# Kernel tuning notes

Measured on AMD Instinct MI355X. Metric: run time of the kernel, lower is better.

The kernel has to match this reference:

```python
import jax, jax.numpy as jnp
import numpy as np

B, N, H, D, L = 2, 256, 256, 64, 6  # batch, pocket atoms, hidden dim, atom feat dim, EGNN layers


def _lin(x, w, b):
    return x @ w + b


def setup_inputs() -> dict:
    key = jax.random.key(0)
    ks = iter(jax.random.split(key, 64))

    def w(shape, s=0.05):
        return jax.random.normal(next(ks), shape, jnp.float32) * s

    inp = {
        'pocket_coords': jax.random.normal(next(ks), (B, N, 3), jnp.float32),
        'pocket_features': jax.random.normal(next(ks), (B, N, D), jnp.float32),
        't': jax.random.uniform(next(ks), (B,), jnp.float32, 0.0, 1000.0),
        'pe_w1': w((3 + D, H)), 'pe_b1': w((H,)),
        'pe_w2': w((H, H)), 'pe_b2': w((H,)),
        'pe_w3': w((H, H)), 'pe_b3': w((H,)),
        'te_w1': w((1, H)), 'te_b1': w((H,)),
        'te_w2': w((H, H)), 'te_b2': w((H,)),
        'ln_g': jnp.ones((L, H), jnp.float32), 'ln_b': jnp.zeros((L, H), jnp.float32),
        'ew1': w((L, 2 * H + 1, H)), 'eb1': w((L, H)),
        'ew2': w((L, H, H)), 'eb2': w((L, H)),
        'cw1': w((L, H, H)), 'cb1': w((L, H)),
        'cw2': w((L, H, 1)), 'cb2': w((L, 1)),
        'nw1': w((L, 2 * H, H)), 'nb1': w((L, H)),
        'nw2': w((L, H, H)), 'nb2': w((L, H)),
        'dec_w1': w((H, H)), 'dec_b1': w((H,)),
        'dec_w2': w((H, H)), 'dec_b2': w((H,)),
        'dec_w3': w((H, 3)), 'dec_b3': w((3,)),
    }
    return inp


def reference(pocket_coords, pocket_features, t,
              pe_w1, pe_b1, pe_w2, pe_b2, pe_w3, pe_b3,
              te_w1, te_b1, te_w2, te_b2,
              ln_g, ln_b,
              ew1, eb1, ew2, eb2,
              cw1, cb1, cw2, cb2,
              nw1, nb1, nw2, nb2,
              dec_w1, dec_b1, dec_w2, dec_b2, dec_w3, dec_b3):
    relu, silu = jax.nn.relu, jax.nn.silu

    # --- pocket encoder (residual MLP; in_dim 67 != H so no skip; dropout = identity at eval)
    pin = jnp.concatenate([pocket_coords, pocket_features], axis=-1)  # [B,N,3+D]
    h = relu(_lin(pin, pe_w1, pe_b1))
    h = relu(_lin(h, pe_w2, pe_b2))
    h = relu(_lin(h, pe_w3, pe_b3))

    # --- time embedding, broadcast over atoms
    te = relu(_lin(t[:, None], te_w1, te_b1))
    te = _lin(te, te_w2, te_b2)  # [B,H]
    h = h + te[:, None, :]

    # --- 6-layer dense EGNN (all-pairs), norm_feats=True -> LayerNorm on h per layer
    x = pocket_coords
    for l in range(L):
        h_in = h
        mu = h.mean(-1, keepdims=True)
        hc = h - mu
        hn = hc / jnp.sqrt((hc * hc).mean(-1, keepdims=True) + 1e-5) * ln_g[l] + ln_b[l]
        rel = x[:, :, None, :] - x[:, None, :, :]            # [B,N,N,3]
        d2 = jnp.sum(rel * rel, axis=-1, keepdims=True)      # [B,N,N,1]
        hi = jnp.broadcast_to(hn[:, :, None, :], (B, N, N, H))
        hj = jnp.broadcast_to(hn[:, None, :, :], (B, N, N, H))
        eij = jnp.concatenate([hi, hj, d2], axis=-1)         # [B,N,N,2H+1]
        m = silu(_lin(eij, ew1[l], eb1[l]))
        m = silu(_lin(m, ew2[l], eb2[l]))                    # [B,N,N,H] messages
        cw = _lin(silu(_lin(m, cw1[l], cb1[l])), cw2[l], cb2[l])  # [B,N,N,1]
        x = x + jnp.mean(rel * cw, axis=2)                   # equivariant coord update
        magg = jnp.sum(m, axis=2)                            # [B,N,H] aggregated messages
        u = silu(_lin(jnp.concatenate([hn, magg], axis=-1), nw1[l], nb1[l]))
        h = h_in + _lin(u, nw2[l], nb2[l])                   # residual node update

    # --- decoder (residual MLP, dims equal so skip applies before final projection)
    o = relu(_lin(h, dec_w1, dec_b1))
    o = relu(_lin(o, dec_w2, dec_b2)) + h
    return _lin(o, dec_w3, dec_b3)                           # predicted noise [B,N,3]
```

## Files before the change

kernel.cpp:

```cpp
#include <hip/hip_runtime.h>
#include <math.h>

static constexpr int NB = 2, NN = 256, HH = 256, DD = 64, LL = 6;
static constexpr int RN = NB * NN * HH;
static constexpr int SROWB = 528;

typedef __attribute__((ext_vector_type(8))) short bf16x8;
typedef __attribute__((ext_vector_type(4))) float f32x4;
typedef __attribute__((ext_vector_type(4))) float float4v;
typedef __attribute__((ext_vector_type(4))) unsigned int u32x4;

__device__ __forceinline__ float fsilu(float v) {
    return v * __builtin_amdgcn_rcpf(1.0f + __expf(-v));
}
__device__ __forceinline__ unsigned short f2bf(float f) {
    union { float f; unsigned int u; } x; x.f = f;
    unsigned int r = x.u + 0x7fffu + ((x.u >> 16) & 1u);
    return (unsigned short)(r >> 16);
}
__device__ __forceinline__ float bitsf(unsigned int u) {
    union { float f; unsigned int u; } x; x.u = u; return x.f;
}
__device__ __forceinline__ float bflo(unsigned int w) { return bitsf(w << 16); }
__device__ __forceinline__ float bfhi(unsigned int w) { return bitsf(w & 0xffff0000u); }
__device__ __forceinline__ unsigned int cvtpk(float lo, float hi) {
    unsigned int w;
    asm("v_cvt_pk_bf16_f32 %0, %1, %2" : "=v"(w) : "v"(lo), "v"(hi));
    return w;
}

__global__ void k_convert(const float* __restrict__ ew2, const float* __restrict__ cw1,
                          unsigned short* __restrict__ ew2P, unsigned short* __restrict__ cw1P) {
    int g = blockIdx.x * blockDim.x + threadIdx.x;
    if (g >= LL * 8192) return;
    int l = g >> 13;
    int r = g & 8191;
    int lane = r & 63;
    int fidx = r >> 6;
    int ks = fidx >> 4;
    int wv = (fidx >> 1) & 7;
    int ct = fidx & 1;
    int col = wv * 32 + ct * 16 + (lane & 15);
    int k0 = ks * 32 + (lane >> 4) * 8;
    #pragma unroll
    for (int e = 0; e < 8; ++e) {
        ew2P[(size_t)g * 8 + e] = f2bf(ew2[((size_t)l * HH + k0 + e) * HH + col]);
        cw1P[(size_t)g * 8 + e] = f2bf(cw1[((size_t)l * HH + k0 + e) * HH + col]);
    }
}

__global__ void k_convert2(const float* __restrict__ nw1, const float* __restrict__ nw2,
                           const float* __restrict__ ew1,
                           unsigned short* __restrict__ nw1B, unsigned short* __restrict__ nw2B,
                           unsigned short* __restrict__ ew1B) {
    int idx = blockIdx.x * blockDim.x + threadIdx.x;
    if (idx >= LL * 131072) return;
    int l = idx >> 17;
    int r = idx & 131071;
    int c = r >> 8, col = r & 255;
    int dst = (l << 17) + ((c >> 1) << 9) + (col << 1) + (c & 1);
    nw1B[dst] = f2bf(nw1[(size_t)l * 131072 + c * 256 + col]);
    ew1B[dst] = f2bf(ew1[(size_t)l * 131328 + c * 256 + col]);
    if (r < 65536) {
        int d2 = (l << 16) + ((c >> 1) << 9) + (col << 1) + (c & 1);
        nw2B[d2] = f2bf(nw2[(size_t)l * 65536 + c * 256 + col]);
    }
}

__global__ __launch_bounds__(256) void k_encoder(
    const float* __restrict__ coords, const float* __restrict__ feats, const float* __restrict__ t,
    const float* __restrict__ pw1, const float* __restrict__ pb1,
    const float* __restrict__ pw2, const float* __restrict__ pb2,
    const float* __restrict__ pw3, const float* __restrict__ pb3,
    const float* __restrict__ tw1, const float* __restrict__ tb1,
    const float* __restrict__ tw2, const float* __restrict__ tb2,
    float* __restrict__ h, float* __restrict__ x) {
    __shared__ float spinT[68][2];
    __shared__ float shaT[HH][2];
    __shared__ float shbT[HH][2];
    __shared__ float ste1[HH];
    int tid = threadIdx.x;
    int base = blockIdx.x * 2;
    int b = base / NN;

    #pragma unroll
    for (int r = 0; r < 2; ++r) {
        int row = base + r;
        if (tid < 3) spinT[tid][r] = coords[row * 3 + tid];
        if (tid < DD) spinT[3 + tid][r] = feats[row * DD + tid];
    }
    float tv = t[b];
    ste1[tid] = fmaxf(tv * tw1[tid] + tb1[tid], 0.0f);
    if (tid < 6) {
        int r = tid / 3, c = tid % 3;
        x[(base + r) * 3 + c] = coords[(base + r) * 3 + c];
    }
    __syncthreads();

    float a0 = pb1[tid], a1 = a0;
    for (int c = 0; c < 67; ++c) {
        float w = pw1[c * HH + tid];
        float2 s = *(const float2*)&spinT[c][0];
        a0 += s.x * w; a1 += s.y * w;
    }
    shaT[tid][0] = fmaxf(a0, 0.f); shaT[tid][1] = fmaxf(a1, 0.f);
    __syncthreads();
    a0 = pb2[tid]; a1 = a0;
    for (int c = 0; c < HH; ++c) {
        float w = pw2[c * HH + tid];
        float2 s = *(const float2*)&shaT[c][0];
        a0 += s.x * w; a1 += s.y * w;
    }
    shbT[tid][0] = fmaxf(a0, 0.f); shbT[tid][1] = fmaxf(a1, 0.f);
    __syncthreads();
    a0 = pb3[tid]; a1 = a0;
    float te = tb2[tid];
    for (int c = 0; c < HH; ++c) {
        float w = pw3[c * HH + tid];
        float2 s = *(const float2*)&shbT[c][0];
        a0 += s.x * w; a1 += s.y * w;
        te += ste1[c] * tw2[c * HH + tid];
    }
    h[(base + 0) * HH + tid] = fmaxf(a0, 0.f) + te;
    h[(base + 1) * HH + tid] = fmaxf(a1, 0.f) + te;
}

__global__ __launch_bounds__(256) void k_ln_aiaj(
    const float* __restrict__ h, const float* __restrict__ g, const float* __restrict__ bta,
    const unsigned int* __restrict__ ew1w, const float* __restrict__ eb1l,
    float* __restrict__ hn, float* __restrict__ Ai, unsigned short* __restrict__ AjB) {
    __shared__ float shnT[HH][2];
    int tid = threadIdx.x, wv = tid >> 6, lane = tid & 63;
    int base = blockIdx.x * 2;

    if (wv < 2) {
        int row = base + wv;
        float v[4];
        #pragma unroll
        for (int q = 0; q < 4; ++q) v[q] = h[row * HH + lane + 64 * q];
        float s = v[0] + v[1] + v[2] + v[3];
        #pragma unroll
        for (int m = 1; m < 64; m <<= 1) s += __shfl_xor(s, m);
        float mu = s * (1.0f / HH);
        float var = 0.f;
        #pragma unroll
        for (int q = 0; q < 4; ++q) { v[q] -= mu; var += v[q] * v[q]; }
        #pragma unroll
        for (int m = 1; m < 64; m <<= 1) var += __shfl_xor(var, m);
        float rstd = rsqrtf(var * (1.0f / HH) + 1e-5f);
        #pragma unroll
        for (int q = 0; q < 4; ++q) {
            int k = lane + 64 * q;
            float hv = v[q] * rstd * g[k] + bta[k];
            shnT[k][wv] = hv;
            hn[row * HH + k] = hv;
        }
    }
    __syncthreads();

    float ai0a = eb1l[tid], ai1a = ai0a, ai0b = 0.f, ai1b = 0.f;
    float aj0a = 0.f, aj1a = 0.f, aj0b = 0.f, aj1b = 0.f;
    #pragma unroll 4
    for (int c2 = 0; c2 < 128; c2 += 2) {
        unsigned int wipA = ew1w[c2 * 256 + tid];
        unsigned int wjpA = ew1w[(128 + c2) * 256 + tid];
        unsigned int wipB = ew1w[(c2 + 1) * 256 + tid];
        unsigned int wjpB = ew1w[(129 + c2) * 256 + tid];
        float4 sA = *(const float4*)&shnT[c2 * 2][0];
        float4 sB = *(const float4*)&shnT[c2 * 2 + 2][0];
        ai0a += sA.x * bflo(wipA) + sA.z * bfhi(wipA);
        ai1a += sA.y * bflo(wipA) + sA.w * bfhi(wipA);
        aj0a += sA.x * bflo(wjpA) + sA.z * bfhi(wjpA);
        aj1a += sA.y * bflo(wjpA) + sA.w * bfhi(wjpA);
        ai0b += sB.x * bflo(wipB) + sB.z * bfhi(wipB);
        ai1b += sB.y * bflo(wipB) + sB.w * bfhi(wipB);
        aj0b += sB.x * bflo(wjpB) + sB.z * bfhi(wjpB);
        aj1b += sB.y * bflo(wjpB) + sB.w * bfhi(wjpB);
    }
    Ai[(base + 0) * HH + tid] = ai0a + ai0b; AjB[(base + 0) * HH + tid] = f2bf(aj0a + aj0b);
    Ai[(base + 1) * HH + tid] = ai1a + ai1b; AjB[(base + 1) * HH + tid] = f2bf(aj1a + aj1b);
}

__global__ __launch_bounds__(512, 1) void k_edge(
    const float* __restrict__ x, const float* __restrict__ Ai, const unsigned short* __restrict__ AjB,
    const float* __restrict__ wd, const float* __restrict__ eb2v,
    const unsigned short* __restrict__ ew2P, const unsigned short* __restrict__ cw1P,
    const float* __restrict__ cb1v, const float* __restrict__ cw2v, const float* __restrict__ cb2p,
    float* __restrict__ h, float* __restrict__ hn,
    float* __restrict__ xnext, float* __restrict__ Ainext, unsigned short* __restrict__ AjBnext,
    const unsigned int* __restrict__ nw1w, const float* __restrict__ nb1l,
    const unsigned int* __restrict__ nw2w, const float* __restrict__ nb2l,
    const float* __restrict__ gamv, const float* __restrict__ betv,
    const unsigned int* __restrict__ ew1wn, const float* __restrict__ eb1n,
    int has_ln) {
    __shared__ float cwpart[8][128];
    __shared__ float smagg2[2][256];
    __shared__ __attribute__((aligned(16))) char s_tile[128 * SROWB];
    __shared__ __attribute__((aligned(16))) char m_tile[128 * SROWB];

    int tid = threadIdx.x, wv = tid >> 6, lane = tid & 63;
    int g4 = lane >> 4, l15 = lane & 15;
    int colbase = wv * 32;
    int ni0 = blockIdx.x * 2;
    int ni1 = ni0 + 1;
    int b = ni0 >> 8;
    int bbase = b * NN;
    int bthr = ((wv << 7) + lane) << 3;
    int k0p = (tid & 31) << 3;

    float wdv[8];
    {
        float4v w0 = *(const float4v*)(wd + k0p);
        float4v w1 = *(const float4v*)(wd + k0p + 4);
        #pragma unroll
        for (int e = 0; e < 4; ++e) { wdv[e] = w0[e]; wdv[4 + e] = w1[e]; }
    }
    float eb2r[2], cb1r[2], cw2r[2];
    #pragma unroll
    for (int ct = 0; ct < 2; ++ct) {
        int col = colbase + ct * 16 + l15;
        eb2r[ct] = eb2v[col]; cb1r[ct] = cb1v[col]; cw2r[ct] = cw2v[col];
    }
    float cb2 = cb2p[0];

    bf16x8 Bew[8][2], Bcw[8][2];
    #pragma unroll
    for (int ks = 0; ks < 8; ++ks) {
        #pragma unroll
        for (int ct = 0; ct < 2; ++ct) {
            Bew[ks][ct] = *(const bf16x8*)(ew2P + (ks << 13) + (ct << 9) + bthr);
            Bcw[ks][ct] = *(const bf16x8*)(cw1P + (ks << 13) + (ct << 9) + bthr);
        }
    }

    char* p1w = s_tile + ((tid >> 5) * SROWB + k0p * 2);
    const char* aA = s_tile + (l15 * SROWB + g4 * 16);
    const char* aM = m_tile + (l15 * SROWB + g4 * 16);
    char* mwA = m_tile + ((g4 * 4) * SROWB + (colbase + l15) * 2);

    #pragma unroll 1
    for (int ir = 0; ir < 2; ++ir) {
        int ni = ni0 + ir;
        float aiv[8];
        {
            float4v a0 = *(const float4v*)(Ai + (size_t)ni * HH + k0p);
            float4v a1 = *(const float4v*)(Ai + (size_t)ni * HH + k0p + 4);
            #pragma unroll
            for (int e = 0; e < 4; ++e) { aiv[e] = a0[e]; aiv[4 + e] = a1[e]; }
        }
        float xi0 = x[ni * 3 + 0], xi1 = x[ni * 3 + 1], xi2 = x[ni * 3 + 2];
        float mgv[2] = {0.f, 0.f};
        float xd0 = 0.f, xd1 = 0.f, xd2 = 0.f;

        #pragma unroll 1
        for (int jc = 0; jc < 2; ++jc) {
            int j0 = jc * 128;
            __syncthreads();

            #pragma unroll
            for (int it = 0; it < 8; ++it) {
                int row = it * 16 + (tid >> 5);
                int j = bbase + j0 + row;
                float rx = xi0 - x[j * 3 + 0];
                float ry = xi1 - x[j * 3 + 1];
                float rz = xi2 - x[j * 3 + 2];
                float d2v = rx * rx + ry * ry + rz * rz;
                u32x4 ajw = *(const u32x4*)(AjB + ((size_t)j * HH + k0p));
                unsigned int uw0, uw1, uw2, uw3;
                uw0 = cvtpk(fsilu(aiv[0] + bflo(ajw[0]) + d2v * wdv[0]), fsilu(aiv[1] + bfhi(ajw[0]) + d2v * wdv[1]));
                uw1 = cvtpk(fsilu(aiv[2] + bflo(ajw[1]) + d2v * wdv[2]), fsilu(aiv[3] + bfhi(ajw[1]) + d2v * wdv[3]));
                uw2 = cvtpk(fsilu(aiv[4] + bflo(ajw[2]) + d2v * wdv[4]), fsilu(aiv[5] + bfhi(ajw[2]) + d2v * wdv[5]));
                uw3 = cvtpk(fsilu(aiv[6] + bflo(ajw[3]) + d2v * wdv[6]), fsilu(aiv[7] + bfhi(ajw[3]) + d2v * wdv[7]));
                u32x4 sv = {uw0, uw1, uw2, uw3};
                *reinterpret_cast<u32x4*>(p1w + it * 16 * SROWB) = sv;
            }
            __syncthreads();

            #pragma unroll 1
            for (int rh = 0; rh < 4; ++rh) {
                f32x4 acc[2][2];
                acc[0][0] = (f32x4){0.f,0.f,0.f,0.f}; acc[0][1] = (f32x4){0.f,0.f,0.f,0.f};
                acc[1][0] = (f32x4){0.f,0.f,0.f,0.f}; acc[1][1] = (f32x4){0.f,0.f,0.f,0.f};
                const char* aBase = aA + rh * 32 * SROWB;
                #pragma unroll
                for (int ks = 0; ks < 8; ++ks) {
                    bf16x8 a0 = *reinterpret_cast<const bf16x8*>(aBase + ks * 64);
                    bf16x8 a1 = *reinterpret_cast<const bf16x8*>(aBase + 16 * SROWB + ks * 64);
                    acc[0][0] = __builtin_amdgcn_mfma_f32_16x16x32_bf16(a0, Bew[ks][0], acc[0][0], 0, 0, 0);
                    acc[0][1] = __builtin_amdgcn_mfma_f32_16x16x32_bf16(a0, Bew[ks][1], acc[0][1], 0, 0, 0);
                    acc[1][0] = __builtin_amdgcn_mfma_f32_16x16x32_bf16(a1, Bew[ks][0], acc[1][0], 0, 0, 0);
                    acc[1][1] = __builtin_amdgcn_mfma_f32_16x16x32_bf16(a1, Bew[ks][1], acc[1][1], 0, 0, 0);
                }
                char* mw = mwA + rh * 32 * SROWB;
                #pragma unroll
                for (int rt = 0; rt < 2; ++rt) {
                    #pragma unroll
                    for (int r = 0; r < 4; ++r) {
                        float v0 = fsilu(acc[rt][0][r] + eb2r[0]);
                        float v1 = fsilu(acc[rt][1][r] + eb2r[1]);
                        mgv[0] += v0; mgv[1] += v1;
                        unsigned int w = cvtpk(v0, v1);
                        char* p = mw + (rt * 16 + r) * SROWB;
                        *reinterpret_cast<unsigned short*>(p) = (unsigned short)w;
                        *reinterpret_cast<unsigned short*>(p + 32) = (unsigned short)(w >> 16);
                    }
                }
            }
            __syncthreads();

            #pragma unroll 1
            for (int rh = 0; rh < 4; ++rh) {
                f32x4 acc[2][2];
                acc[0][0] = (f32x4){0.f,0.f,0.f,0.f}; acc[0][1] = (f32x4){0.f,0.f,0.f,0.f};
                acc[1][0] = (f32x4){0.f,0.f,0.f,0.f}; acc[1][1] = (f32x4){0.f,0.f,0.f,0.f};
                const char* aBase = aM + rh * 32 * SROWB;
                #pragma unroll
                for (int ks = 0; ks < 8; ++ks) {
                    bf16x8 a0 = *reinterpret_cast<const bf16x8*>(aBase + ks * 64);
                    bf16x8 a1 = *reinterpret_cast<const bf16x8*>(aBase + 16 * SROWB + ks * 64);
                    acc[0][0] = __builtin_amdgcn_mfma_f32_16x16x32_bf16(a0, Bcw[ks][0], acc[0][0], 0, 0, 0);
                    acc[0][1] = __builtin_amdgcn_mfma_f32_16x16x32_bf16(a0, Bcw[ks][1], acc[0][1], 0, 0, 0);
                    acc[1][0] = __builtin_amdgcn_mfma_f32_16x16x32_bf16(a1, Bcw[ks][0], acc[1][0], 0, 0, 0);
                    acc[1][1] = __builtin_amdgcn_mfma_f32_16x16x32_bf16(a1, Bcw[ks][1], acc[1][1], 0, 0, 0);
                }
                float rs[8];
                #pragma unroll
                for (int q = 0; q < 8; ++q) rs[q] = 0.f;
                #pragma unroll
                for (int ct = 0; ct < 2; ++ct) {
                    #pragma unroll
                    for (int rt = 0; rt < 2; ++rt)
                        #pragma unroll
                        for (int r = 0; r < 4; ++r)
                            rs[rt * 4 + r] += fsilu(acc[rt][ct][r] + cb1r[ct]) * cw2r[ct];
                }
                #pragma unroll
                for (int m = 1; m <= 8; m <<= 1)
                    #pragma unroll
                    for (int q = 0; q < 8; ++q) rs[q] += __shfl_xor(rs[q], m);
                if (l15 == 0) {
                    #pragma unroll
                    for (int rt = 0; rt < 2; ++rt)
                        #pragma unroll
                        for (int r = 0; r < 4; ++r)
                            cwpart[wv][rh * 32 + rt * 16 + g4 * 4 + r] = rs[rt * 4 + r];
                }
            }
            __syncthreads();
            if (tid < 64) {
                #pragma unroll 1
                for (int q = 0; q < 2; ++q) {
                    int lr = q * 64 + tid;
                    float cwv = cb2;
                    #pragma unroll
                    for (int w = 0; w < 8; ++w) cwv += cwpart[w][lr];
                    int j = bbase + j0 + lr;
                    float p0 = (xi0 - x[j * 3 + 0]) * cwv;
                    float p1 = (xi1 - x[j * 3 + 1]) * cwv;
                    float p2 = (xi2 - x[j * 3 + 2]) * cwv;
                    #pragma unroll
                    for (int m = 1; m < 64; m <<= 1) {
                        p0 += __shfl_xor(p0, m); p1 += __shfl_xor(p1, m); p2 += __shfl_xor(p2, m);
                    }
                    xd0 += p0; xd1 += p1; xd2 += p2;
                }
            }
        }

        #pragma unroll
        for (int ct = 0; ct < 2; ++ct) {
            mgv[ct] += __shfl_xor(mgv[ct], 16);
            mgv[ct] += __shfl_xor(mgv[ct], 32);
        }
        if (lane < 16) {
            smagg2[ir][colbase + lane] = mgv[0];
            smagg2[ir][colbase + 16 + lane] = mgv[1];
        }
        if (has_ln && tid == 0) {
            xnext[ni * 3 + 0] = xi0 + xd0 * (1.0f / NN);
            xnext[ni * 3 + 1] = xi1 + xd1 * (1.0f / NN);
            xnext[ni * 3 + 2] = xi2 + xd2 * (1.0f / NN);
        }
    }
    __syncthreads();

    float* s2T   = (float*)s_tile;
    float* part0 = (float*)(s_tile + 4096);
    float* part1 = (float*)(s_tile + 6144);
    float* suT   = (float*)(s_tile + 8192);
    float* shrow = (float*)(s_tile + 10240);
    float* shnT  = (float*)(s_tile + 12288);

    if (tid < 256) {
        s2T[tid * 2 + 0] = hn[(size_t)ni0 * HH + tid];
        s2T[tid * 2 + 1] = hn[(size_t)ni1 * HH + tid];
        s2T[(HH + tid) * 2 + 0] = smagg2[0][tid];
        s2T[(HH + tid) * 2 + 1] = smagg2[1][tid];
    }
    __syncthreads();
    {
        int col = tid & 255, kh = tid >> 8;
        const unsigned int* w = nw1w + (kh * 128) * 256;
        const float* sv = s2T + kh * 512;
        float p0a = 0.f, p1a = 0.f, p0b = 0.f, p1b = 0.f;
        #pragma unroll 4
        for (int c2 = 0; c2 < 128; c2 += 2) {
            unsigned int wpA = w[c2 * 256 + col];
            unsigned int wpB = w[(c2 + 1) * 256 + col];
            float4 sA = *(const float4*)&sv[c2 * 4];
            float4 sB = *(const float4*)&sv[c2 * 4 + 4];
            p0a += sA.x * bflo(wpA) + sA.z * bfhi(wpA);
            p1a += sA.y * bflo(wpA) + sA.w * bfhi(wpA);
            p0b += sB.x * bflo(wpB) + sB.z * bfhi(wpB);
            p1b += sB.y * bflo(wpB) + sB.w * bfhi(wpB);
        }
        part0[tid] = p0a + p0b; part1[tid] = p1a + p1b;
    }
    __syncthreads();
    if (tid < 256) {
        float bb = nb1l[tid];
        suT[tid * 2 + 0] = fsilu(part0[tid] + part0[256 + tid] + bb);
        suT[tid * 2 + 1] = fsilu(part1[tid] + part1[256 + tid] + bb);
    }
    __syncthreads();
    {
        int col = tid & 255, kh = tid >> 8;
        const unsigned int* w = nw2w + (kh * 64) * 256;
        const float* sv = suT + kh * 256;
        float p0a = 0.f, p1a = 0.f, p0b = 0.f, p1b = 0.f;
        #pragma unroll 4
        for (int c2 = 0; c2 < 64; c2 += 2) {
            unsigned int wpA = w[c2 * 256 + col];
            unsigned int wpB = w[(c2 + 1) * 256 + col];
            float4 sA = *(const float4*)&sv[c2 * 4];
            float4 sB = *(const float4*)&sv[c2 * 4 + 4];
            p0a += sA.x * bflo(wpA) + sA.z * bfhi(wpA);
            p1a += sA.y * bflo(wpA) + sA.w * bfhi(wpA);
            p0b += sB.x * bflo(wpB) + sB.z * bfhi(wpB);
            p1b += sB.y * bflo(wpB) + sB.w * bfhi(wpB);
        }
        part0[tid] = p0a + p0b; part1[tid] = p1a + p1b;
    }
    __syncthreads();
    if (tid < 256) {
        float bb = nb2l[tid];
        float h0v = h[(size_t)ni0 * HH + tid] + part0[tid] + part0[256 + tid] + bb;
        float h1v = h[(size_t)ni1 * HH + tid] + part1[tid] + part1[256 + tid] + bb;
        h[(size_t)ni0 * HH + tid] = h0v;
        h[(size_t)ni1 * HH + tid] = h1v;
        shrow[tid * 2 + 0] = h0v;
        shrow[tid * 2 + 1] = h1v;
    }
    __syncthreads();
    if (!has_ln) return;

    if (wv < 2) {
        float v[4];
        #pragma unroll
        for (int q = 0; q < 4; ++q) v[q] = shrow[(lane + 64 * q) * 2 + wv];
        float s = v[0] + v[1] + v[2] + v[3];
        #pragma unroll
        for (int m = 1; m < 64; m <<= 1) s += __shfl_xor(s, m);
        float mu = s * (1.0f / HH);
        float var = 0.f;
        #pragma unroll
        for (int q = 0; q < 4; ++q) { v[q] -= mu; var += v[q] * v[q]; }
        #pragma unroll
        for (int m = 1; m < 64; m <<= 1) var += __shfl_xor(var, m);
        float rstd = rsqrtf(var * (1.0f / HH) + 1e-5f);
        #pragma unroll
        for (int q = 0; q < 4; ++q) {
            int k = lane + 64 * q;
            float hv = v[q] * rstd * gamv[k] + betv[k];
            shnT[k * 2 + wv] = hv;
            hn[(size_t)(ni0 + wv) * HH + k] = hv;
        }
    }
    __syncthreads();
    {
        int col = tid & 255, hf = tid >> 8;
        const unsigned int* w = ew1wn + (hf * 128) * 256;
        float p0a = (hf == 0) ? eb1n[col] : 0.f;
        float p1a = p0a;
        float p0b = 0.f, p1b = 0.f;
        #pragma unroll 4
        for (int c2 = 0; c2 < 128; c2 += 2) {
            unsigned int wpA = w[c2 * 256 + col];
            unsigned int wpB = w[(c2 + 1) * 256 + col];
            float4 sA = *(const float4*)&shnT[c2 * 4];
            float4 sB = *(const float4*)&shnT[c2 * 4 + 4];
            p0a += sA.x * bflo(wpA) + sA.z * bfhi(wpA);
            p1a += sA.y * bflo(wpA) + sA.w * bfhi(wpA);
            p0b += sB.x * bflo(wpB) + sB.z * bfhi(wpB);
            p1b += sB.y * bflo(wpB) + sB.w * bfhi(wpB);
        }
        float p0 = p0a + p0b, p1 = p1a + p1b;
        if (hf == 0) {
            Ainext[(size_t)ni0 * HH + col] = p0;
            Ainext[(size_t)ni1 * HH + col] = p1;
        } else {
            AjBnext[(size_t)ni0 * HH + col] = f2bf(p0);
            AjBnext[(size_t)ni1 * HH + col] = f2bf(p1);
        }
    }
}

__global__ __launch_bounds__(256) void k_decoder(
    const float* __restrict__ h,
    const float* __restrict__ dw1, const float* __restrict__ db1,
    const float* __restrict__ dw2, const float* __restrict__ db2,
    const float* __restrict__ dw3, const float* __restrict__ db3,
    float* __restrict__ out) {
    __shared__ float shT[HH][2];
    __shared__ float so1T[HH][2];
    __shared__ float so2T[HH][2];
    int tid = threadIdx.x;
    int base = blockIdx.x * 2;
    #pragma unroll
    for (int r = 0; r < 2; ++r) shT[tid][r] = h[(base + r) * HH + tid];
    __syncthreads();
    float a0 = db1[tid], a1 = a0;
    for (int c = 0; c < HH; ++c) {
        float w = dw1[c * HH + tid];
        float2 s = *(const float2*)&shT[c][0];
        a0 += s.x * w; a1 += s.y * w;
    }
    so1T[tid][0] = fmaxf(a0, 0.f); so1T[tid][1] = fmaxf(a1, 0.f);
    __syncthreads();
    a0 = db2[tid]; a1 = a0;
    for (int c = 0; c < HH; ++c) {
        float w = dw2[c * HH + tid];
        float2 s = *(const float2*)&so1T[c][0];
        a0 += s.x * w; a1 += s.y * w;
    }
    so2T[tid][0] = fmaxf(a0, 0.f) + shT[tid][0];
    so2T[tid][1] = fmaxf(a1, 0.f) + shT[tid][1];
    __syncthreads();
    if (tid < 6) {
        int r = tid / 3, c = tid % 3;
        float acc = db3[c];
        for (int k = 0; k < HH; ++k) acc += so2T[k][r] * dw3[k * 3 + c];
        out[(base + r) * 3 + c] = acc;
    }
}

extern "C" void kernel_launch(void* const* d_in, const int* in_sizes, int n_in,
                              void* d_out, int out_size, void* d_ws, size_t ws_size,
                              hipStream_t stream) {
    const float* coords = (const float*)d_in[0];
    const float* feats  = (const float*)d_in[1];
    const float* t      = (const float*)d_in[2];
    const float* pe_w1  = (const float*)d_in[3];  const float* pe_b1 = (const float*)d_in[4];
    const float* pe_w2  = (const float*)d_in[5];  const float* pe_b2 = (const float*)d_in[6];
    const float* pe_w3  = (const float*)d_in[7];  const float* pe_b3 = (const float*)d_in[8];
    const float* te_w1  = (const float*)d_in[9];  const float* te_b1 = (const float*)d_in[10];
    const float* te_w2  = (const float*)d_in[11]; const float* te_b2 = (const float*)d_in[12];
    const float* ln_g   = (const float*)d_in[13]; const float* ln_b  = (const float*)d_in[14];
    const float* ew1    = (const float*)d_in[15]; const float* eb1   = (const float*)d_in[16];
    const float* ew2    = (const float*)d_in[17]; const float* eb2   = (const float*)d_in[18];
    const float* cw1    = (const float*)d_in[19]; const float* cb1   = (const float*)d_in[20];
    const float* cw2    = (const float*)d_in[21]; const float* cb2   = (const float*)d_in[22];
    const float* nw1    = (const float*)d_in[23]; const float* nb1   = (const float*)d_in[24];
    const float* nw2    = (const float*)d_in[25]; const float* nb2   = (const float*)d_in[26];
    const float* dec_w1 = (const float*)d_in[27]; const float* dec_b1 = (const float*)d_in[28];
    const float* dec_w2 = (const float*)d_in[29]; const float* dec_b2 = (const float*)d_in[30];
    const float* dec_w3 = (const float*)d_in[31]; const float* dec_b3 = (const float*)d_in[32];

    float* ws = (float*)d_ws;
    float* h    = ws;
    float* hn   = ws + RN;
    float* Ai0  = ws + 2 * RN;
    float* Ai1  = ws + 3 * RN;
    float* xb0  = ws + 4 * RN;
    float* xb1  = ws + 4 * RN + 2048;
    unsigned short* Aj0  = (unsigned short*)(ws + 4 * RN + 4096);
    unsigned short* Aj1  = Aj0 + RN;
    unsigned short* ew2P = Aj1 + RN;
    unsigned short* cw1P = ew2P + LL * HH * HH;
    unsigned short* nw1B = cw1P + LL * HH * HH;
    unsigned short* ew1B = nw1B + LL * 2 * HH * HH;
    unsigned short* nw2B = ew1B + LL * 2 * HH * HH;

    k_convert<<<(LL * 8192 + 511) / 512, 512, 0, stream>>>(ew2, cw1, ew2P, cw1P);
    k_convert2<<<(LL * 131072 + 255) / 256, 256, 0, stream>>>(nw1, nw2, ew1, nw1B, nw2B, ew1B);
    k_encoder<<<NB * NN / 2, 256, 0, stream>>>(coords, feats, t,
        pe_w1, pe_b1, pe_w2, pe_b2, pe_w3, pe_b3, te_w1, te_b1, te_w2, te_b2, h, xb0);
    k_ln_aiaj<<<NB * NN / 2, 256, 0, stream>>>(h, ln_g, ln_b,
        (const unsigned int*)ew1B, eb1, hn, Ai0, Aj0);

    for (int l = 0; l < LL; ++l) {
        const float* xin = (l & 1) ? xb1 : xb0;
        float* xout      = (l & 1) ? xb0 : xb1;
        const float* AiIn = (l & 1) ? Ai1 : Ai0;
        float* AiOut      = (l & 1) ? Ai0 : Ai1;
        const unsigned short* AjIn = (l & 1) ? Aj1 : Aj0;
        unsigned short* AjOut      = (l & 1) ? Aj0 : Aj1;
        int ln = (l + 1 < LL) ? (l + 1) : LL - 1;
        k_edge<<<NB * NN / 2, 512, 0, stream>>>(xin, AiIn, AjIn,
            ew1 + ((size_t)l * 513 + 512) * HH, eb2 + l * HH,
            ew2P + (size_t)l * HH * HH, cw1P + (size_t)l * HH * HH,
            cb1 + l * HH, cw2 + l * HH, cb2 + l,
            h, hn, xout, AiOut, AjOut,
            (const unsigned int*)(nw1B + (size_t)l * 2 * HH * HH), nb1 + l * HH,
            (const unsigned int*)(nw2B + (size_t)l * HH * HH), nb2 + l * HH,
            ln_g + ln * HH, ln_b + ln * HH,
            (const unsigned int*)(ew1B + (size_t)ln * 2 * HH * HH), eb1 + ln * HH,
            (l + 1 < LL) ? 1 : 0);
    }

    k_decoder<<<NB * NN / 2, 256, 0, stream>>>(h, dec_w1, dec_b1, dec_w2, dec_b2,
                                               dec_w3, dec_b3, (float*)d_out);
}
```

Baseline: 514.3 us.

## Double-buffer edge tiles in 64-row chunks to overlap build with MFMA

The edge kernel now processes neighbours in four 64-row chunks instead of two 128-row chunks. It uses two ping-pong LDS buffers so the next chunk's first-layer SiLU tile is built right after the current chunk's ew2 MFMAs, before the barrier. The goal is to hide the VALU and global-load work of building the input tile behind the tensor-core work and drop one barrier per chunk. In exchange there are more loop iterations and barriers overall, plus a smaller m-tile and shorter coordinate-reduction steps.

```diff
diff --git a/kernel.cpp b/kernel.cpp
--- a/kernel.cpp
+++ b/kernel.cpp
@@ -193,10 +193,11 @@
     const float* __restrict__ gamv, const float* __restrict__ betv,
     const unsigned int* __restrict__ ew1wn, const float* __restrict__ eb1n,
     int has_ln) {
-    __shared__ float cwpart[8][128];
+    __shared__ float cwpart[8][64];
     __shared__ float smagg2[2][256];
-    __shared__ __attribute__((aligned(16))) char s_tile[128 * SROWB];
-    __shared__ __attribute__((aligned(16))) char m_tile[128 * SROWB];
+    __shared__ __attribute__((aligned(16))) char s_t0[64 * SROWB];
+    __shared__ __attribute__((aligned(16))) char s_t1[64 * SROWB];
+    __shared__ __attribute__((aligned(16))) char m_t[64 * SROWB];
 
     int tid = threadIdx.x, wv = tid >> 6, lane = tid & 63;
     int g4 = lane >> 4, l15 = lane & 15;
@@ -233,11 +234,6 @@
         }
     }
 
-    char* p1w = s_tile + ((tid >> 5) * SROWB + k0p * 2);
-    const char* aA = s_tile + (l15 * SROWB + g4 * 16);
-    const char* aM = m_tile + (l15 * SROWB + g4 * 16);
-    char* mwA = m_tile + ((g4 * 4) * SROWB + (colbase + l15) * 2);
-
     #pragma unroll 1
     for (int ir = 0; ir < 2; ++ir) {
         int ni = ni0 + ir;
@@ -252,15 +248,12 @@
         float mgv[2] = {0.f, 0.f};
         float xd0 = 0.f, xd1 = 0.f, xd2 = 0.f;
 
-        #pragma unroll 1
-        for (int jc = 0; jc < 2; ++jc) {
-            int j0 = jc * 128;
-            __syncthreads();
-
+        auto phase1 = [&](int kk, char* dst) {
+            char* pw = dst + ((tid >> 5) * SROWB + k0p * 2);
             #pragma unroll
-            for (int it = 0; it < 8; ++it) {
+            for (int it = 0; it < 4; ++it) {
                 int row = it * 16 + (tid >> 5);
-                int j = bbase + j0 + row;
+                int j = bbase + kk * 64 + row;
                 float rx = xi0 - x[j * 3 + 0];
                 float ry = xi1 - x[j * 3 + 1];
                 float rz = xi2 - x[j * 3 + 2];
@@ -272,16 +265,25 @@
                 uw2 = cvtpk(fsilu(aiv[4] + bflo(ajw[2]) + d2v * wdv[4]), fsilu(aiv[5] + bfhi(ajw[2]) + d2v * wdv[5]));
                 uw3 = cvtpk(fsilu(aiv[6] + bflo(ajw[3]) + d2v * wdv[6]), fsilu(aiv[7] + bfhi(ajw[3]) + d2v * wdv[7]));
                 u32x4 sv = {uw0, uw1, uw2, uw3};
-                *reinterpret_cast<u32x4*>(p1w + it * 16 * SROWB) = sv;
+                *reinterpret_cast<u32x4*>(pw + it * 16 * SROWB) = sv;
             }
-            __syncthreads();
-
-            #pragma unroll 1
-            for (int rh = 0; rh < 4; ++rh) {
+        };
+
+        __syncthreads();
+        phase1(0, s_t0);
+        __syncthreads();
+
+        #pragma unroll 1
+        for (int k = 0; k < 4; ++k) {
+            const char* sb = (k & 1) ? s_t1 : s_t0;
+            char* snext    = (k & 1) ? s_t0 : s_t1;
+
+            #pragma unroll
+            for (int rh = 0; rh < 2; ++rh) {
                 f32x4 acc[2][2];
                 acc[0][0] = (f32x4){0.f,0.f,0.f,0.f}; acc[0][1] = (f32x4){0.f,0.f,0.f,0.f};
                 acc[1][0] = (f32x4){0.f,0.f,0.f,0.f}; acc[1][1] = (f32x4){0.f,0.f,0.f,0.f};
-                const char* aBase = aA + rh * 32 * SROWB;
+                const char* aBase = sb + (l15 * SROWB + g4 * 16) + rh * 32 * SROWB;
                 #pragma unroll
                 for (int ks = 0; ks < 8; ++ks) {
                     bf16x8 a0 = *reinterpret_cast<const bf16x8*>(aBase + ks * 64);
@@ -291,7 +293,7 @@
                     acc[1][0] = __builtin_amdgcn_mfma_f32_16x16x32_bf16(a1, Bew[ks][0], acc[1][0], 0, 0, 0);
                     acc[1][1] = __builtin_amdgcn_mfma_f32_16x16x32_bf16(a1, Bew[ks][1], acc[1][1], 0, 0, 0);
                 }
-                char* mw = mwA + rh * 32 * SROWB;
+                char* mw = m_t + ((g4 * 4) * SROWB + (colbase + l15) * 2) + rh * 32 * SROWB;
                 #pragma unroll
                 for (int rt = 0; rt < 2; ++rt) {
                     #pragma unroll
@@ -306,14 +308,15 @@
                     }
                 }
             }
+            if (k < 3) phase1(k + 1, snext);
             __syncthreads();
 
-            #pragma unroll 1
-            for (int rh = 0; rh < 4; ++rh) {
+            #pragma unroll
+            for (int rh = 0; rh < 2; ++rh) {
                 f32x4 acc[2][2];
                 acc[0][0] = (f32x4){0.f,0.f,0.f,0.f}; acc[0][1] = (f32x4){0.f,0.f,0.f,0.f};
                 acc[1][0] = (f32x4){0.f,0.f,0.f,0.f}; acc[1][1] = (f32x4){0.f,0.f,0.f,0.f};
-                const char* aBase = aM + rh * 32 * SROWB;
+                const char* aBase = m_t + (l15 * SROWB + g4 * 16) + rh * 32 * SROWB;
                 #pragma unroll
                 for (int ks = 0; ks < 8; ++ks) {
                     bf16x8 a0 = *reinterpret_cast<const bf16x8*>(aBase + ks * 64);
@@ -348,22 +351,18 @@
             }
             __syncthreads();
             if (tid < 64) {
-                #pragma unroll 1
-                for (int q = 0; q < 2; ++q) {
-                    int lr = q * 64 + tid;
-                    float cwv = cb2;
-                    #pragma unroll
-                    for (int w = 0; w < 8; ++w) cwv += cwpart[w][lr];
-                    int j = bbase + j0 + lr;
-                    float p0 = (xi0 - x[j * 3 + 0]) * cwv;
-                    float p1 = (xi1 - x[j * 3 + 1]) * cwv;
-                    float p2 = (xi2 - x[j * 3 + 2]) * cwv;
-                    #pragma unroll
-                    for (int m = 1; m < 64; m <<= 1) {
-                        p0 += __shfl_xor(p0, m); p1 += __shfl_xor(p1, m); p2 += __shfl_xor(p2, m);
-                    }
-                    xd0 += p0; xd1 += p1; xd2 += p2;
+                float cwv = cb2;
+                #pragma unroll
+                for (int w = 0; w < 8; ++w) cwv += cwpart[w][tid];
+                int j = bbase + k * 64 + tid;
+                float p0 = (xi0 - x[j * 3 + 0]) * cwv;
+                float p1 = (xi1 - x[j * 3 + 1]) * cwv;
+                float p2 = (xi2 - x[j * 3 + 2]) * cwv;
+                #pragma unroll
+                for (int m = 1; m < 64; m <<= 1) {
+                    p0 += __shfl_xor(p0, m); p1 += __shfl_xor(p1, m); p2 += __shfl_xor(p2, m);
                 }
+                xd0 += p0; xd1 += p1; xd2 += p2;
             }
         }
 
@@ -384,12 +383,12 @@
     }
     __syncthreads();
 
-    float* s2T   = (float*)s_tile;
-    float* part0 = (float*)(s_tile + 4096);
-    float* part1 = (float*)(s_tile + 6144);
-    float* suT   = (float*)(s_tile + 8192);
-    float* shrow = (float*)(s_tile + 10240);
-    float* shnT  = (float*)(s_tile + 12288);
+    float* s2T   = (float*)s_t0;
+    float* part0 = (float*)(s_t0 + 4096);
+    float* part1 = (float*)(s_t0 + 6144);
+    float* suT   = (float*)(s_t0 + 8192);
+    float* shrow = (float*)(s_t0 + 10240);
+    float* shnT  = (float*)(s_t0 + 12288);
 
     if (tid < 256) {
         s2T[tid * 2 + 0] = hn[(size_t)ni0 * HH + tid];
```

Result: slower. 578.4 us (+12.5%).
